# Kernel tuning notes

Hardware: AMD Instinct MI355X
Metric: run time of the kernel (lower is better)

The kernel has to match this reference:

```python
import jax, jax.numpy as jnp
import numpy as np

E = 128          # out_embedding_size
N = 128          # n_atoms
B = 512          # batch
CUTOFF = 5.0
LOG_STD_MIN, LOG_STD_MAX = -20.0, 2.0


def shifted_softplus(x):
    return jax.nn.softplus(x) - jnp.log(2.0).astype(x.dtype)


def cosine_cutoff(r):
    # SchNetPack CosineCutoff: 0.5*(cos(pi*r/rc)+1) for r < rc, else 0
    return 0.5 * (jnp.cos(r * (jnp.pi / CUTOFF)) + 1.0) * (r < CUTOFF).astype(r.dtype)


def setup_inputs() -> dict:
    key = jax.random.key(0)
    ks = jax.random.split(key, 8)
    kx = jax.random.normal(ks[0], (B, N, 2 * E + 1), dtype=jnp.float32)
    positions = jax.random.uniform(ks[1], (B, N, 3), dtype=jnp.float32) * 10.0
    # prefix-ones atoms mask (molecules padded at the end), 64..128 real atoms
    num_atoms = jax.random.randint(ks[2], (B,), 64, N + 1)
    atoms_mask = (jnp.arange(N)[None, :] < num_atoms[:, None]).astype(jnp.float32)
    eval_actions = jax.random.normal(ks[3], (B, N, 3), dtype=jnp.float32) * 0.1
    Wx = jax.random.normal(ks[4], (E, E), dtype=jnp.float32) / np.sqrt(E)
    bx = jnp.zeros((E,), dtype=jnp.float32)
    Wk = jax.random.normal(ks[5], (E, E), dtype=jnp.float32) / np.sqrt(E)
    bk = jnp.zeros((E,), dtype=jnp.float32)
    return {
        "kx": kx, "positions": positions, "atoms_mask": atoms_mask,
        "action_scale": jnp.float32(1.0), "eval_actions": eval_actions,
        "Wx": Wx, "bx": bx, "Wk": Wk, "bk": bk,
    }


def reference(kx, positions, atoms_mask, action_scale, eval_actions, Wx, bx, Wk, bk):
    kx = kx * atoms_mask[..., None]
    # P[b,i,j] = pos[b,j] - pos[b,i]
    P = positions[:, None, :, :] - positions[:, :, None, :]
    # safe norm: tiny eps inside sqrt so grads are finite on the zero diagonal
    r_ij = jnp.sqrt(jnp.sum(P * P, axis=-1) + 1e-16)
    P = P / (r_ij[..., None] + 1e-8)

    x = kx[..., :E]
    k = kx[..., E:2 * E]
    actions_log_std = kx[..., 2 * E:]  # [B,N,1]

    x = shifted_softplus(x) @ Wx.T + bx
    k = jax.nn.relu(k) @ Wk.T + bk

    inv_sqrt_e = 1.0 / jnp.sqrt(jnp.float32(E))
    x = jnp.einsum('bie,bje->bij', x, x) * inv_sqrt_e
    x = (r_ij - x) * 0.5
    k = jnp.einsum('bie,bje->bij', k, k) * inv_sqrt_e
    f = x * k

    # neighborhood mask: first num_atoms rows/cols are 1 (vectorized get_nbh_mask)
    counts = jnp.sum(atoms_mask, axis=-1)              # [B]
    idx = jnp.arange(N, dtype=counts.dtype)
    valid = (idx[None, :] < counts[:, None]).astype(f.dtype)   # [B,N]
    nbh_mask = valid[:, :, None] * valid[:, None, :]           # [B,N,N]

    fcut = cosine_cutoff(r_ij) * nbh_mask
    # summation_order='to' -> sum over dim 1
    actions_mean = jnp.sum(P * (f * fcut)[..., None], axis=1)  # [B,N,3]

    # limit_actions: tanh renormalization
    actions_norm = jnp.sqrt(jnp.sum(actions_mean * actions_mean, axis=-1) + 1e-16) + 1e-8
    actions_mean = actions_mean / actions_norm[..., None] * jnp.tanh(actions_norm)[..., None]

    # training path with eval_actions supplied
    actions_log_std = jnp.clip(actions_log_std, LOG_STD_MIN, LOG_STD_MAX)
    mu = actions_mean * action_scale
    sigma = jnp.exp(actions_log_std) * action_scale   # [B,N,1], broadcasts
    actions = eval_actions
    log_prob = (-0.5 * jnp.square((actions - mu) / sigma)
                - jnp.log(sigma)
                - 0.5 * jnp.log(2.0 * jnp.pi))
    log_prob = log_prob * atoms_mask[..., None]
    log_prob = jnp.sum(log_prob, axis=(1, 2))[:, None]  # [B,1]

    actions = actions * atoms_mask[..., None]
    return actions, log_prob
```

## Files before the change

### kernel.cpp

```cpp
#include <hip/hip_runtime.h>
#include <math.h>

#define EDIM 128
#define NATOM 128
#define NBATCH 512
#define THREADS 512
#define ROWLEN 257

typedef __attribute__((ext_vector_type(8))) short bf16x8;
typedef __attribute__((ext_vector_type(4))) float f32x4;
typedef __attribute__((ext_vector_type(4))) unsigned short u16x4;

__device__ __forceinline__ unsigned short f2bf(float f) {
    unsigned u = __float_as_uint(f);
    u += 0x7FFFu + ((u >> 16) & 1u);
    return (unsigned short)(u >> 16);
}
__device__ __forceinline__ unsigned short cvt1(float x) {
    unsigned r;
    asm("v_cvt_pk_bf16_f32 %0, %1, %1" : "=v"(r) : "v"(x));
    return (unsigned short)r;
}
__device__ __forceinline__ float fast_ssp(float x) {
    return fmaxf(x, 0.f) + __logf(1.f + __expf(-fabsf(x))) - 0.69314718055994531f;
}
__device__ __forceinline__ int swzp(int row, int cbyte, int phase) {
    return row * 256 + ((cbyte ^ phase) ^ ((row & 7) << 4));
}

#define PH 0
#define QH 32768

__global__ void wcvt_kernel(const float* __restrict__ Wx,
                            const float* __restrict__ Wk,
                            unsigned short* __restrict__ ws) {
    int g = blockIdx.x * 256 + threadIdx.x;
    const float* src = (g < 16384) ? Wx : Wk;
    ws[g] = f2bf(src[g & 16383]);
}

__global__ void __launch_bounds__(THREADS, 4)
gen_actions_kernel(const float* __restrict__ kx,
                   const float* __restrict__ pos,
                   const float* __restrict__ mask,
                   const float* __restrict__ scale_ptr,
                   const float* __restrict__ evala,
                   const float* __restrict__ bx,
                   const float* __restrict__ bk,
                   const unsigned short* __restrict__ ws,
                   float* __restrict__ out)
{
    extern __shared__ char lds[];
    __shared__ float posXs[NATOM], posYs[NATOM], posZs[NATOM], lsBs[NATOM];
    __shared__ float amBs[NATOM * 3];
    __shared__ float redBs[2];
    __shared__ int   cntBs[2];

    const int b = blockIdx.x;
    const int t = threadIdx.x;
    const int lane = t & 63;
    const int w = t >> 6;
    const int wrb = w >> 2;
    const int wc = w & 3;
    const int l15 = lane & 15;
    const int l4  = lane >> 4;

    if (t < NATOM) {
        float m = mask[b * NATOM + t];
        unsigned long long bal = __ballot(m > 0.5f);
        if ((t & 63) == 0) cntBs[t >> 6] = __popcll(bal);
        const float* p = pos + ((size_t)b * NATOM + t) * 3;
        posXs[t] = p[0]; posYs[t] = p[1]; posZs[t] = p[2];
        lsBs[t] = kx[(size_t)b * (NATOM * ROWLEN) + t * ROWLEN + 2 * EDIM];
    }
    if (t < NATOM * 3) amBs[t] = 0.f;

    {
        const float* kb = kx + (size_t)b * (NATOM * ROWLEN);
        #pragma unroll 4
        for (int j = 0; j < 32; ++j) {
            const int row = (j * 8 + w) & 127;
            const bool isX = (j < 16);
            const float* src = kb + row * ROWLEN + (isX ? 0 : 128);
            float x0 = src[lane];
            float x1 = src[lane + 64];
            float a0 = isX ? fast_ssp(x0) : fmaxf(x0, 0.f);
            float a1 = isX ? fast_ssp(x1) : fmaxf(x1, 0.f);
            char* base = lds + (isX ? PH : QH);
            const int phase = isX ? 0 : 64;
            *(unsigned short*)(base + swzp(row, lane * 2, phase)) = cvt1(a0);
            *(unsigned short*)(base + swzp(row, (lane + 64) * 2, phase)) = cvt1(a1);
        }
    }
    __syncthreads();
    const int count = cntBs[0] + cntBs[1];

    const int n0 = wc * 32;
    const bool nact = (n0 < count);

    #define GEMM_MAT(MAT, PLANE, PHASE, WSOFF, BIAS)                                    \
    {                                                                                   \
        u16x4 pk[2][2][2];                                                              \
        if (nact) {                                                                     \
            const char* act = lds + PLANE;                                              \
            const unsigned short* WH = ws + WSOFF;                                      \
            f32x4 acc[2][2][2] = {};                                                    \
            for (int ks = 0; ks < 4; ++ks) {                                            \
                const int e0 = ks * 32 + l4 * 8;                                        \
                bf16x8 ah[2];                                                           \
                _Pragma("unroll")                                                       \
                for (int nf = 0; nf < 2; ++nf)                                          \
                    ah[nf] = *(const bf16x8*)(act + swzp(n0 + nf * 16 + l15, e0 * 2, PHASE)); \
                _Pragma("unroll")                                                       \
                for (int p = 0; p < 2; ++p) {                                           \
                    _Pragma("unroll")                                                   \
                    for (int mf = 0; mf < 2; ++mf) {                                    \
                        int orow = (wrb + 2 * p) * 32 + mf * 16 + l15;                  \
                        bf16x8 wh = *(const bf16x8*)(WH + orow * 128 + e0);             \
                        _Pragma("unroll")                                               \
                        for (int nf = 0; nf < 2; ++nf)                                  \
                            acc[p][mf][nf] = __builtin_amdgcn_mfma_f32_16x16x32_bf16(wh, ah[nf], acc[p][mf][nf], 0, 0, 0); \
                    }                                                                   \
                }                                                                       \
            }                                                                           \
            _Pragma("unroll")                                                           \
            for (int p = 0; p < 2; ++p)                                                 \
                _Pragma("unroll")                                                       \
                for (int mf = 0; mf < 2; ++mf) {                                        \
                    int ob = (wrb + 2 * p) * 32 + mf * 16 + l4 * 4;                     \
                    f32x4 b4 = *(const f32x4*)(BIAS + ob);                              \
                    _Pragma("unroll")                                                   \
                    for (int nf = 0; nf < 2; ++nf) {                                    \
                        u16x4 hs;                                                       \
                        _Pragma("unroll")                                               \
                        for (int r = 0; r < 4; ++r) hs[r] = cvt1(acc[p][mf][nf][r] + b4[r]); \
                        pk[p][mf][nf] = hs;                                             \
                    }                                                                   \
                }                                                                       \
        }                                                                               \
        __syncthreads();                      \
        if (nact) {                                                                     \
            _Pragma("unroll")                                                           \
            for (int p = 0; p < 2; ++p)                                                 \
                _Pragma("unroll")                                                       \
                for (int mf = 0; mf < 2; ++mf) {                                        \
                    int ob2 = ((wrb + 2 * p) * 32 + mf * 16 + l4 * 4) * 2;              \
                    _Pragma("unroll")                                                   \
                    for (int nf = 0; nf < 2; ++nf) {                                    \
                        int jrow = n0 + nf * 16 + l15;                                  \
                        *(u16x4*)(lds + PLANE + swzp(jrow, ob2, PHASE)) = pk[p][mf][nf]; \
                    }                                                                   \
                }                                                                       \
        }                                                                               \
    }

    GEMM_MAT(0, PH, 0,  0,     bx)
    GEMM_MAT(1, QH, 64, 16384, bk)
    __syncthreads();

    const int n0g = n0;
    if (n0g < count) {
        f32x4 gx[2][2][2] = {}, gk[2][2][2] = {};
        for (int ks = 0; ks < 4; ++ks) {
            const int e0b = (ks * 32 + l4 * 8) * 2;
            bf16x8 bX[2], bK[2];
            #pragma unroll
            for (int nf = 0; nf < 2; ++nf) {
                bX[nf] = *(const bf16x8*)(lds + PH + swzp(n0g + nf * 16 + l15, e0b, 0));
                bK[nf] = *(const bf16x8*)(lds + QH + swzp(n0g + nf * 16 + l15, e0b, 64));
            }
            #pragma unroll
            for (int p = 0; p < 2; ++p) {
                const int m0g = (wrb + 2 * p) * 32;
                if (m0g < count) {
                    #pragma unroll
                    for (int mf = 0; mf < 2; ++mf) {
                        int irow = m0g + mf * 16 + l15;
                        bf16x8 aX = *(const bf16x8*)(lds + PH + swzp(irow, e0b, 0));
                        bf16x8 aK = *(const bf16x8*)(lds + QH + swzp(irow, e0b, 64));
                        #pragma unroll
                        for (int nf = 0; nf < 2; ++nf) {
                            gx[p][mf][nf] = __builtin_amdgcn_mfma_f32_16x16x32_bf16(aX, bX[nf], gx[p][mf][nf], 0, 0, 0);
                            gk[p][mf][nf] = __builtin_amdgcn_mfma_f32_16x16x32_bf16(aK, bK[nf], gk[p][mf][nf], 0, 0, 0);
                        }
                    }
                }
            }
        }
        const float inv_e = 0.08838834764831845f;
        #pragma unroll
        for (int nf = 0; nf < 2; ++nf) {
            const int j = n0g + nf * 16 + l15;
            const bool jvalid = (j < count);
            const float pjx = posXs[j], pjy = posYs[j], pjz = posZs[j];
            float amx = 0.f, amy = 0.f, amz = 0.f;
            #pragma unroll
            for (int p = 0; p < 2; ++p) {
                const int m0g = (wrb + 2 * p) * 32;
                if (m0g < count) {
                    #pragma unroll
                    for (int mf = 0; mf < 2; ++mf) {
                        #pragma unroll
                        for (int r = 0; r < 4; ++r) {
                            const int i = m0g + mf * 16 + l4 * 4 + r;
                            float dx = pjx - posXs[i];
                            float dy = pjy - posYs[i];
                            float dz = pjz - posZs[i];
                            float r2 = fmaf(dx, dx, fmaf(dy, dy, dz * dz)) + 1e-16f;
                            float rr = sqrtf(r2);
                            bool ok = jvalid && (i < count) && (rr < 5.0f);
                            float fc = ok ? (0.5f * (__cosf(rr * 0.62831853071795865f) + 1.f)) : 0.f;
                            float xs = fmaf(gx[p][mf][nf][r], -0.044194173824159216f, rr * 0.5f);
                            float fv = xs * (gk[p][mf][nf][r] * inv_e) * fc;
                            float wgt = fv / (rr + 1e-8f);
                            amx = fmaf(dx, wgt, amx);
                            amy = fmaf(dy, wgt, amy);
                            amz = fmaf(dz, wgt, amz);
                        }
                    }
                }
            }
            amx += __shfl_xor(amx, 16); amx += __shfl_xor(amx, 32);
            amy += __shfl_xor(amy, 16); amy += __shfl_xor(amy, 32);
            amz += __shfl_xor(amz, 16); amz += __shfl_xor(amz, 32);
            if (l4 == 0 && jvalid) {
                atomicAdd(&amBs[j * 3 + 0], amx);
                atomicAdd(&amBs[j * 3 + 1], amy);
                atomicAdd(&amBs[j * 3 + 2], amz);
            }
        }
    }
    __syncthreads();

    if (t < 96) {
        f32x4 ev4 = *(const f32x4*)(evala + (size_t)b * 384 + t * 4);
        f32x4 o4;
        #pragma unroll
        for (int c = 0; c < 4; ++c) {
            int atom = (t * 4 + c) / 3;
            o4[c] = (atom < count) ? ev4[c] : 0.f;
        }
        *(f32x4*)(out + (size_t)b * 384 + t * 4) = o4;
    }
    float lp = 0.f;
    if (t < NATOM && t < count) {
        const float* ev = evala + ((size_t)b * NATOM + t) * 3;
        float e0v = ev[0], e1v = ev[1], e2v = ev[2];
        float scale = scale_ptr[0];
        float ax = amBs[t * 3 + 0], ay = amBs[t * 3 + 1], az = amBs[t * 3 + 2];
        float nrm = sqrtf(fmaf(ax, ax, fmaf(ay, ay, az * az)) + 1e-16f) + 1e-8f;
        float qe = __expf(-2.f * nrm);
        float th = (1.f - qe) / (1.f + qe);
        float sc = th / nrm * scale;
        float ls = fminf(fmaxf(lsBs[t], -20.f), 2.f);
        float sig = __expf(ls) * scale;
        float sinv = 1.f / sig;
        float zx = (e0v - ax * sc) * sinv;
        float zy = (e1v - ay * sc) * sinv;
        float zz = (e2v - az * sc) * sinv;
        lp = -0.5f * (zx * zx + zy * zy + zz * zz) - 3.f * __logf(sig)
             - 3.f * 0.91893853320467274f;
    }
    #pragma unroll
    for (int off = 32; off > 0; off >>= 1) lp += __shfl_down(lp, off);
    if (t == 0)  redBs[0] = lp;
    if (t == 64) redBs[1] = lp;
    __syncthreads();
    if (t == 0) out[(size_t)NBATCH * NATOM * 3 + b] = redBs[0] + redBs[1];
}

extern "C" void kernel_launch(void* const* d_in, const int* in_sizes, int n_in,
                              void* d_out, int out_size, void* d_ws, size_t ws_size,
                              hipStream_t stream) {
    const float* kx    = (const float*)d_in[0];
    const float* pos   = (const float*)d_in[1];
    const float* mask  = (const float*)d_in[2];
    const float* scale = (const float*)d_in[3];
    const float* ev    = (const float*)d_in[4];
    const float* Wx    = (const float*)d_in[5];
    const float* bx    = (const float*)d_in[6];
    const float* Wk    = (const float*)d_in[7];
    const float* bk    = (const float*)d_in[8];
    float* out = (float*)d_out;
    unsigned short* ws = (unsigned short*)d_ws;

    hipLaunchKernelGGL(wcvt_kernel, dim3(128), dim3(256), 0, stream, Wx, Wk, ws);

    const size_t shbytes = 65536;
    (void)hipFuncSetAttribute((const void*)gen_actions_kernel,
                              hipFuncAttributeMaxDynamicSharedMemorySize,
                              (int)shbytes);
    hipLaunchKernelGGL(gen_actions_kernel, dim3(NBATCH), dim3(THREADS), shbytes, stream,
                       kx, pos, mask, scale, ev, bx, bk, ws, out);
}
```

Before: 53.09 us.

## Skip padded rows in staging, pack LDS pos, vectorize bf16 stores, fast sqrt/rcp

The staging loop now computes the atom count per wave and skips kx rows beyond the count rounded up to 32. It also processes the x and k halves of each row together and writes packed bf16 pairs with one 32-bit LDS store. Positions and log-std are packed into one float4 LDS array, and the epilogue loop is reordered so each i-position load serves both column fragments. Exact sqrt and division are replaced with hardware sqrt and reciprocal intrinsics, which trades a little precision for fewer instructions.

After: 53.72 us. No clear change (+1.2%).

```diff
diff --git a/kernel.cpp b/kernel.cpp
--- a/kernel.cpp
+++ b/kernel.cpp
@@ -20,6 +20,11 @@
     unsigned r;
     asm("v_cvt_pk_bf16_f32 %0, %1, %1" : "=v"(r) : "v"(x));
     return (unsigned short)r;
+}
+__device__ __forceinline__ unsigned cvt2(float a0, float a1) {
+    unsigned r;
+    asm("v_cvt_pk_bf16_f32 %0, %1, %2" : "=v"(r) : "v"(a0), "v"(a1));
+    return r;
 }
 __device__ __forceinline__ float fast_ssp(float x) {
     return fmaxf(x, 0.f) + __logf(1.f + __expf(-fabsf(x))) - 0.69314718055994531f;
@@ -51,7 +56,7 @@
                    float* __restrict__ out)
 {
     extern __shared__ char lds[];
-    __shared__ float posXs[NATOM], posYs[NATOM], posZs[NATOM], lsBs[NATOM];
+    __shared__ f32x4 posQs[NATOM];
     __shared__ float amBs[NATOM * 3];
     __shared__ float redBs[2];
     __shared__ int   cntBs[2];
@@ -70,26 +75,33 @@
         unsigned long long bal = __ballot(m > 0.5f);
         if ((t & 63) == 0) cntBs[t >> 6] = __popcll(bal);
         const float* p = pos + ((size_t)b * NATOM + t) * 3;
-        posXs[t] = p[0]; posYs[t] = p[1]; posZs[t] = p[2];
-        lsBs[t] = kx[(size_t)b * (NATOM * ROWLEN) + t * ROWLEN + 2 * EDIM];
+        f32x4 q;
+        q[0] = p[0]; q[1] = p[1]; q[2] = p[2];
+        q[3] = kx[(size_t)b * (NATOM * ROWLEN) + t * ROWLEN + 2 * EDIM];
+        posQs[t] = q;
     }
     if (t < NATOM * 3) amBs[t] = 0.f;
 
     {
+        float mA = mask[b * NATOM + lane];
+        float mB = mask[b * NATOM + 64 + lane];
+        int cnt = __popcll(__ballot(mA > 0.5f)) + __popcll(__ballot(mB > 0.5f));
+        const int cnt32 = (cnt + 31) & ~31;
         const float* kb = kx + (size_t)b * (NATOM * ROWLEN);
         #pragma unroll 4
-        for (int j = 0; j < 32; ++j) {
-            const int row = (j * 8 + w) & 127;
-            const bool isX = (j < 16);
-            const float* src = kb + row * ROWLEN + (isX ? 0 : 128);
-            float x0 = src[lane];
-            float x1 = src[lane + 64];
-            float a0 = isX ? fast_ssp(x0) : fmaxf(x0, 0.f);
-            float a1 = isX ? fast_ssp(x1) : fmaxf(x1, 0.f);
-            char* base = lds + (isX ? PH : QH);
-            const int phase = isX ? 0 : 64;
-            *(unsigned short*)(base + swzp(row, lane * 2, phase)) = cvt1(a0);
-            *(unsigned short*)(base + swzp(row, (lane + 64) * 2, phase)) = cvt1(a1);
+        for (int rr2 = 0; rr2 < 16; ++rr2) {
+            const int row = rr2 * 8 + w;
+            if (row < cnt32) {
+                const float* src = kb + row * ROWLEN;
+                float x0 = src[2 * lane];
+                float x1 = src[2 * lane + 1];
+                float y0 = src[128 + 2 * lane];
+                float y1 = src[128 + 2 * lane + 1];
+                unsigned pa = cvt2(fast_ssp(x0), fast_ssp(x1));
+                unsigned pc = cvt2(fmaxf(y0, 0.f), fmaxf(y1, 0.f));
+                *(unsigned*)(lds + PH + swzp(row, 4 * lane, 0))  = pa;
+                *(unsigned*)(lds + QH + swzp(row, 4 * lane, 64)) = pc;
+            }
         }
     }
     __syncthreads();
@@ -188,42 +200,54 @@
             }
         }
         const float inv_e = 0.08838834764831845f;
+        float am[2][3] = {};
+        f32x4 pj4[2];
+        bool jv[2];
         #pragma unroll
         for (int nf = 0; nf < 2; ++nf) {
             const int j = n0g + nf * 16 + l15;
-            const bool jvalid = (j < count);
-            const float pjx = posXs[j], pjy = posYs[j], pjz = posZs[j];
-            float amx = 0.f, amy = 0.f, amz = 0.f;
-            #pragma unroll
-            for (int p = 0; p < 2; ++p) {
-                const int m0g = (wrb + 2 * p) * 32;
-                if (m0g < count) {
+            jv[nf] = (j < count);
+            pj4[nf] = posQs[j];
+        }
+        #pragma unroll
+        for (int p = 0; p < 2; ++p) {
+            const int m0g = (wrb + 2 * p) * 32;
+            if (m0g < count) {
+                #pragma unroll
+                for (int mf = 0; mf < 2; ++mf) {
                     #pragma unroll
-                    for (int mf = 0; mf < 2; ++mf) {
+                    for (int r = 0; r < 4; ++r) {
+                        const int i = m0g + mf * 16 + l4 * 4 + r;
+                        f32x4 pi4 = posQs[i];
+                        const bool iv = (i < count);
                         #pragma unroll
-                        for (int r = 0; r < 4; ++r) {
-                            const int i = m0g + mf * 16 + l4 * 4 + r;
-                            float dx = pjx - posXs[i];
-                            float dy = pjy - posYs[i];
-                            float dz = pjz - posZs[i];
+                        for (int nf = 0; nf < 2; ++nf) {
+                            float dx = pj4[nf][0] - pi4[0];
+                            float dy = pj4[nf][1] - pi4[1];
+                            float dz = pj4[nf][2] - pi4[2];
                             float r2 = fmaf(dx, dx, fmaf(dy, dy, dz * dz)) + 1e-16f;
-                            float rr = sqrtf(r2);
-                            bool ok = jvalid && (i < count) && (rr < 5.0f);
+                            float rr = __builtin_amdgcn_sqrtf(r2);
+                            bool ok = jv[nf] && iv && (rr < 5.0f);
                             float fc = ok ? (0.5f * (__cosf(rr * 0.62831853071795865f) + 1.f)) : 0.f;
                             float xs = fmaf(gx[p][mf][nf][r], -0.044194173824159216f, rr * 0.5f);
                             float fv = xs * (gk[p][mf][nf][r] * inv_e) * fc;
-                            float wgt = fv / (rr + 1e-8f);
-                            amx = fmaf(dx, wgt, amx);
-                            amy = fmaf(dy, wgt, amy);
-                            amz = fmaf(dz, wgt, amz);
+                            float wgt = fv * __builtin_amdgcn_rcpf(rr + 1e-8f);
+                            am[nf][0] = fmaf(dx, wgt, am[nf][0]);
+                            am[nf][1] = fmaf(dy, wgt, am[nf][1]);
+                            am[nf][2] = fmaf(dz, wgt, am[nf][2]);
                         }
                     }
                 }
             }
+        }
+        #pragma unroll
+        for (int nf = 0; nf < 2; ++nf) {
+            float amx = am[nf][0], amy = am[nf][1], amz = am[nf][2];
             amx += __shfl_xor(amx, 16); amx += __shfl_xor(amx, 32);
             amy += __shfl_xor(amy, 16); amy += __shfl_xor(amy, 32);
             amz += __shfl_xor(amz, 16); amz += __shfl_xor(amz, 32);
-            if (l4 == 0 && jvalid) {
+            if (l4 == 0 && jv[nf]) {
+                const int j = n0g + nf * 16 + l15;
                 atomicAdd(&amBs[j * 3 + 0], amx);
                 atomicAdd(&amBs[j * 3 + 1], amy);
                 atomicAdd(&amBs[j * 3 + 2], amz);
@@ -247,12 +271,13 @@
         const float* ev = evala + ((size_t)b * NATOM + t) * 3;
         float e0v = ev[0], e1v = ev[1], e2v = ev[2];
         float scale = scale_ptr[0];
+        f32x4 q = posQs[t];
         float ax = amBs[t * 3 + 0], ay = amBs[t * 3 + 1], az = amBs[t * 3 + 2];
         float nrm = sqrtf(fmaf(ax, ax, fmaf(ay, ay, az * az)) + 1e-16f) + 1e-8f;
         float qe = __expf(-2.f * nrm);
         float th = (1.f - qe) / (1.f + qe);
         float sc = th / nrm * scale;
-        float ls = fminf(fmaxf(lsBs[t], -20.f), 2.f);
+        float ls = fminf(fmaxf(q[3], -20.f), 2.f);
         float sig = __expf(ls) * scale;
         float sinv = 1.f / sig;
         float zx = (e0v - ax * sc) * sinv;
```
